# Performance work log

Measured on AMD Instinct MI355X. Metric: run time of the kernel, lower is better.

## Reference

```python
import jax, jax.numpy as jnp
import numpy as np

N_NODES = 50000
N_EDGES = 1600000
F_IN = 128
F_OUT = 64
K_ATT = 4


def setup_inputs() -> dict:
    key = jax.random.key(0)
    ks = jax.random.split(key, 12)
    s_in = 1.0 / np.sqrt(F_IN)
    s_2o = 1.0 / np.sqrt(2 * F_OUT)
    x = jax.random.normal(ks[0], (N_NODES, F_IN), dtype=jnp.float32)
    src = jax.random.randint(ks[1], (N_EDGES,), 0, N_NODES)
    dst = jax.random.randint(ks[2], (N_EDGES,), 0, N_NODES)
    Wv = jax.random.normal(ks[3], (F_IN, F_OUT), dtype=jnp.float32) * s_in
    bv = jnp.zeros((F_OUT,), dtype=jnp.float32)
    Wn = jax.random.normal(ks[4], (F_IN, F_OUT), dtype=jnp.float32) * s_in
    bn = jnp.zeros((F_OUT,), dtype=jnp.float32)
    Wt = jax.random.normal(ks[5], (K_ATT, F_IN, F_OUT), dtype=jnp.float32) * s_in
    bt = jnp.zeros((K_ATT, F_OUT), dtype=jnp.float32)
    Wa = jax.random.normal(ks[6], (K_ATT, 2 * F_OUT, F_OUT), dtype=jnp.float32) * s_2o
    ba = jnp.zeros((K_ATT, F_OUT), dtype=jnp.float32)
    return {"x": x, "src": src, "dst": dst, "Wv": Wv, "bv": bv,
            "Wn": Wn, "bn": bn, "Wt": Wt, "bt": bt, "Wa": Wa, "ba": ba}


def _forward(x, src, dst, Wv, bv, Wn, bn, Wt, bt, Wa, ba):
    N = x.shape[0]
    k = Wt.shape[0]
    out = Wv.shape[1]
    # multi-head attention logits, accumulated over heads (mean over k heads)
    att_edge = jnp.zeros((src.shape[0], out), dtype=x.dtype)
    att_self = jnp.zeros((N, out), dtype=x.dtype)
    for i in range(k):  # small fixed head count
        t = x @ Wt[i] + bt[i]                       # [N, out]
        pair_e = jnp.concatenate([t[dst], t[src]], axis=-1)  # [E, 2*out]
        att_edge = att_edge + jax.nn.relu(pair_e @ Wa[i] + ba[i])
        pair_s = jnp.concatenate([t, t], axis=-1)            # [N, 2*out]
        att_self = att_self + jax.nn.relu(pair_s @ Wa[i] + ba[i])
    att_edge = att_edge / k
    att_self = att_self / k
    e_edge = jnp.exp(att_edge)   # [E, out]
    e_self = jnp.exp(att_self)   # [N, out]
    denom = e_self + jax.ops.segment_sum(e_edge, dst, num_segments=N)
    m_self = x @ Wv + bv                  # self message  [N, out]
    m_nb = x[src] @ Wn + bn               # neighbor msgs [E, out]
    num = e_self * m_self + jax.ops.segment_sum(e_edge * m_nb, dst, num_segments=N)
    return jax.nn.relu(num / denom)


def reference(x, src, dst, Wv, bv, Wn, bn, Wt, bt, Wa, ba):
    return _forward(x, src, dst, Wv, bv, Wn, bn, Wt, bt, Wa, ba)
```

## Files before the change

### kernel.cpp

```cpp
#include <hip/hip_runtime.h>
#include <hip/hip_fp16.h>
#include <cstdint>
#include <cstddef>

#define F_IN 128
#define F_OUT 64
#define KH 4
#define CHUNK 4096
#define CAP 12800

typedef _Float16 v8h __attribute__((ext_vector_type(8)));
typedef _Float16 h2v __attribute__((ext_vector_type(2)));
typedef float v4f __attribute__((ext_vector_type(4)));
typedef float v2f __attribute__((ext_vector_type(2)));


__global__ __launch_bounds__(256) void k_part(const int* __restrict__ src,
                                              const int* __restrict__ dst,
                                              int* __restrict__ gcnt,
                                              int* __restrict__ ppack, int E){
  __shared__ int h[256];
  __shared__ int cur[256];
  const int b = blockIdx.x, t = threadIdx.x;
  h[t] = 0; __syncthreads();
  const int base = b*CHUNK;
  #pragma unroll
  for (int it = 0; it < 16; ++it){
    int i = base + it*256 + t;
    if (i < E) atomicAdd(&h[dst[i] >> 8], 1);
  }
  __syncthreads();
  if (h[t] > 0) cur[t] = t*CAP + atomicAdd(&gcnt[t], h[t]);
  __syncthreads();
  #pragma unroll
  for (int it = 0; it < 16; ++it){
    int i = base + it*256 + t;
    if (i < E){
      int d = dst[i];
      int p = atomicAdd(&cur[d >> 8], 1);
      ppack[p] = src[i] | ((d & 255) << 16);
    }
  }
}

__global__ __launch_bounds__(256) void k_fine(const int* __restrict__ ppack,
                                              const int* __restrict__ gcnt,
                                              int* __restrict__ ssrc,
                                              int* __restrict__ beg,
                                              int* __restrict__ endv, int N){
  __shared__ int s_pk[CAP];
  __shared__ int hist[256];
  __shared__ int cur[256];
  const int bkt = blockIdx.x, t = threadIdx.x;
  const int cnt = min(gcnt[bkt], CAP);
  const int b0 = bkt*CAP;
  hist[t] = 0; __syncthreads();
  for (int i = t; i < cnt; i += 256){
    int pk = ppack[b0 + i];
    atomicAdd(&hist[pk >> 16], 1);
    s_pk[i] = pk;
  }
  __syncthreads();
  int v = hist[t];
  cur[t] = v; __syncthreads();
  for (int d = 1; d < 256; d <<= 1){
    int tmp = (t >= d) ? cur[t-d] : 0;
    __syncthreads(); cur[t] += tmp; __syncthreads();
  }
  int excl = cur[t] - v;
  int node = bkt*256 + t;
  if (node < N){ beg[node] = b0 + excl; endv[node] = b0 + excl + v; }
  __syncthreads();
  cur[t] = b0 + excl;
  __syncthreads();
  for (int i = t; i < cnt; i += 256){
    int pk = s_pk[i];
    int p = atomicAdd(&cur[pk >> 16], 1);
    ssrc[p] = pk & 0xFFFF;
  }
}


__device__ __forceinline__ size_t frag_idx(int k, int col){
  int p = col >> 7, n = col & 127;
  int nt = n >> 4, nn = n & 15;
  int kc = k >> 5, q = (k >> 3) & 3, j = k & 7;
  return ((((size_t)(p*8 + nt)*4 + kc)*64) + (nn + q*16))*8 + j;
}

__global__ __launch_bounds__(256) void k_fuse(
  const float* __restrict__ Wt, const float* __restrict__ bt,
  const float* __restrict__ Wa, const float* __restrict__ ba,
  const float* __restrict__ Wv, const float* __restrict__ bv,
  const float* __restrict__ Wn, const float* __restrict__ bn,
  __half* __restrict__ Wfrag, float* __restrict__ bbig)
{
  const int b = blockIdx.x;
  const int t = threadIdx.x;

  if (b >= 8){
    int idx = (b-8)*256 + t;
    int r = idx >> 6, c = idx & 63;
    int colms = 512 + (c&7)*16 + (c>>3);
    int colh  = 512 + (c&7)*16 + 8 + (c>>3);
    Wfrag[frag_idx(r, colms)] = __float2half_rn(Wv[r*64 + c]);
    Wfrag[frag_idx(r, colh)]  = __float2half_rn(Wn[r*64 + c]);
    if (idx < 64){
      bbig[512 + (idx&7)*16 + (idx>>3)]     = bv[idx];
      bbig[512 + (idx&7)*16 + 8 + (idx>>3)] = bn[idx];
    }
    return;
  }

  __shared__ float WaH[64*65];
  const int i = b >> 1, half = b & 1;
  const int c = t & 63, w = t >> 6;

  for (int it = 0; it < 16; ++it){
    int idx = it*256 + t;
    int j = idx >> 6, cc = idx & 63;
    WaH[j*65 + cc] = Wa[i*8192 + (half*64 + j)*64 + cc];
  }
  __syncthreads();

  const int cl = c & 31;
  const int col = (c>>5)*128 + ((cl&1)*4 + i)*16 + (cl>>1) + (half ? 256 : 0);

  if (w == 0){
    const float4* bt4 = (const float4*)(bt + i*64);
    float bias = (half == 0) ? ba[i*64 + c] : 0.f;
    #pragma unroll
    for (int j4 = 0; j4 < 16; ++j4){
      float4 bv4 = bt4[j4];
      bias = fmaf(bv4.x, WaH[(j4*4+0)*65 + c], bias);
      bias = fmaf(bv4.y, WaH[(j4*4+1)*65 + c], bias);
      bias = fmaf(bv4.z, WaH[(j4*4+2)*65 + c], bias);
      bias = fmaf(bv4.w, WaH[(j4*4+3)*65 + c], bias);
    }
    bbig[col] = bias;
  }

  for (int s = 0; s < 32; ++s){
    int r = w*32 + s;
    const float4* wtr = (const float4*)(Wt + i*8192 + r*64);
    float acc = 0.f;
    #pragma unroll
    for (int j4 = 0; j4 < 16; ++j4){
      float4 w4 = wtr[j4];
      acc = fmaf(w4.x, WaH[(j4*4+0)*65 + c], acc);
      acc = fmaf(w4.y, WaH[(j4*4+1)*65 + c], acc);
      acc = fmaf(w4.z, WaH[(j4*4+2)*65 + c], acc);
      acc = fmaf(w4.w, WaH[(j4*4+3)*65 + c], acc);
    }
    Wfrag[frag_idx(r, col)] = __float2half_rn(acc);
  }
}


__global__ __launch_bounds__(256, 4) void k_gemm(
  const float* __restrict__ x, const __half* __restrict__ Wfrag,
  const float* __restrict__ bbig,
  __half* __restrict__ UMS, unsigned char* __restrict__ VH, int N)
{
  __shared__ __half Wl[16384];
  const int t = threadIdx.x;
  const int l = t & 63;
  const int w = __builtin_amdgcn_readfirstlane(t >> 6);
  const int q = l >> 4;
  const int nn = l & 15;
  const int mbase = blockIdx.x*64 + w*16;
  const int m = mbase + nn;
  const int mm = min(m, N-1);

  v8h a[4];
  const float4* xp = (const float4*)(x + (size_t)mm*128);
  #pragma unroll
  for (int kc = 0; kc < 4; ++kc){
    float4 f0 = xp[kc*8 + q*2 + 0];
    float4 f1 = xp[kc*8 + q*2 + 1];
    v8h av;
    av[0]=(_Float16)f0.x; av[1]=(_Float16)f0.y; av[2]=(_Float16)f0.z; av[3]=(_Float16)f0.w;
    av[4]=(_Float16)f1.x; av[5]=(_Float16)f1.y; av[6]=(_Float16)f1.z; av[7]=(_Float16)f1.w;
    a[kc] = av;
  }

  const v8h* Bl = (const v8h*)Wl;

  for (int p = 0; p < 5; ++p){
    __syncthreads();
    {
      const float4* sp = (const float4*)(Wfrag + (size_t)p*16384);
      float4* dp = (float4*)Wl;
      #pragma unroll
      for (int it = 0; it < 8; ++it) dp[it*256 + t] = sp[it*256 + t];
    }
    __syncthreads();

    v4f acc[8];
    #pragma unroll
    for (int nt = 0; nt < 8; ++nt){
      v4f ac = {0.f, 0.f, 0.f, 0.f};
      ac = __builtin_amdgcn_mfma_f32_16x16x32_f16(a[0], Bl[(nt*4+0)*64 + l], ac, 0,0,0);
      ac = __builtin_amdgcn_mfma_f32_16x16x32_f16(a[1], Bl[(nt*4+1)*64 + l], ac, 0,0,0);
      ac = __builtin_amdgcn_mfma_f32_16x16x32_f16(a[2], Bl[(nt*4+2)*64 + l], ac, 0,0,0);
      ac = __builtin_amdgcn_mfma_f32_16x16x32_f16(a[3], Bl[(nt*4+3)*64 + l], ac, 0,0,0);
      acc[nt] = ac;
    }

    float bbv[8];
    #pragma unroll
    for (int nt = 0; nt < 8; ++nt) bbv[nt] = bbig[p*128 + nt*16 + nn];

    #pragma unroll
    for (int r = 0; r < 4; ++r){
      int node = mbase + q*4 + r;
      if (node >= N) continue;
      float vv[8];
      #pragma unroll
      for (int nt = 0; nt < 8; ++nt) vv[nt] = acc[nt][r] + bbv[nt];

      if (p < 2){
        union { float4 f; __half h[8]; } O;
        #pragma unroll
        for (int nt = 0; nt < 8; ++nt) O.h[nt] = __float2half_rn(vv[nt]);
        __half* dstp = UMS + (size_t)node*320 + p*128 + nn*8;
        *(float4*)dstp = O.f;
      } else if (p < 4){
        int w0 = 0, w1 = 0;
        w0 = __builtin_amdgcn_cvt_pk_fp8_f32(vv[0], vv[1], w0, false);
        w0 = __builtin_amdgcn_cvt_pk_fp8_f32(vv[2], vv[3], w0, true);
        w1 = __builtin_amdgcn_cvt_pk_fp8_f32(vv[4], vv[5], w1, false);
        w1 = __builtin_amdgcn_cvt_pk_fp8_f32(vv[6], vv[7], w1, true);
        int2 pkd = make_int2(w0, w1);
        *(int2*)(VH + (size_t)node*384 + (p-2)*128 + nn*8) = pkd;
      } else {
        union { float4 f; __half h[8]; } O;
        #pragma unroll
        for (int nt = 0; nt < 8; ++nt) O.h[nt] = __float2half_rn(vv[nt]);
        if (nn < 8)
          *(float4*)(UMS + (size_t)node*320 + 256 + nn*8) = O.f;
        else
          *(float4*)(VH + (size_t)node*384 + 256 + (nn-8)*16) = O.f;
      }
    }
  }
}


__device__ __forceinline__ float elogit8(float u0,float u1,float u2,float u3, int vd){
  v2f p01 = __builtin_amdgcn_cvt_pk_f32_fp8(vd, false);
  v2f p23 = __builtin_amdgcn_cvt_pk_f32_fp8(vd, true);
  return fmaxf(u0+p01[0],0.f) + fmaxf(u1+p01[1],0.f)
       + fmaxf(u2+p23[0],0.f) + fmaxf(u3+p23[1],0.f);
}

__global__ __launch_bounds__(256) void k_edge(
  const __half* __restrict__ UMS, const unsigned char* __restrict__ VH,
  const int* __restrict__ beg, const int* __restrict__ endv,
  const int* __restrict__ ssrc,
  float* __restrict__ out, int N)
{
  int gid = blockIdx.x * 256 + threadIdx.x;
  int n = __builtin_amdgcn_readfirstlane(gid >> 6);
  int c = threadIdx.x & 63;
  if (n >= N) return;

  const float2* __restrict__ U2 = (const float2*)UMS;

  float u0, u1, u2, u3;
  {
    union { float2 f; __half2 h[2]; } U; U.f = U2[(size_t)n*80 + c];
    u0 = __low2float(U.h[0]); u1 = __high2float(U.h[0]);
    u2 = __low2float(U.h[1]); u3 = __high2float(U.h[1]);
  }
  float ms = __half2float(UMS[(size_t)n*320 + 256 + c]);

  const size_t vo = (size_t)c*4;
  const size_t ho = 256 + (size_t)c*2;

  float num, den;
  {
    int vd = *(const int*)(VH + (size_t)n*384 + vo);
    float es = __expf(0.25f * elogit8(u0,u1,u2,u3, vd));
    den = es; num = es * ms;
  }

  int j = beg[n], end = endv[n];
  for (; j + 16 <= end; j += 16){
    int vd[16]; __half hv[16];
    #pragma unroll
    for (int e = 0; e < 16; ++e){
      int s = ssrc[j+e];
      const unsigned char* r = VH + (size_t)s*384;
      vd[e] = *(const int*)(r + vo);
      hv[e] = *(const __half*)(r + ho);
    }
    float ad = 0.f, an = 0.f;
    #pragma unroll
    for (int e = 0; e < 16; ++e){
      float ee = __expf(0.25f * elogit8(u0,u1,u2,u3, vd[e]));
      ad += ee;
      an = fmaf(ee, __half2float(hv[e]), an);
    }
    den += ad; num += an;
  }
  for (; j + 4 <= end; j += 4){
    int vd[4]; __half hv[4];
    #pragma unroll
    for (int e = 0; e < 4; ++e){
      int s = ssrc[j+e];
      const unsigned char* r = VH + (size_t)s*384;
      vd[e] = *(const int*)(r + vo);
      hv[e] = *(const __half*)(r + ho);
    }
    float ad = 0.f, an = 0.f;
    #pragma unroll
    for (int e = 0; e < 4; ++e){
      float ee = __expf(0.25f * elogit8(u0,u1,u2,u3, vd[e]));
      ad += ee;
      an = fmaf(ee, __half2float(hv[e]), an);
    }
    den += ad; num += an;
  }
  for (; j < end; ++j){
    int s = ssrc[j];
    const unsigned char* r = VH + (size_t)s*384;
    int vdv = *(const int*)(r + vo);
    float hvv = __half2float(*(const __half*)(r + ho));
    float ee = __expf(0.25f * elogit8(u0,u1,u2,u3, vdv));
    den += ee;
    num = fmaf(ee, hvv, num);
  }
  out[(size_t)n*64 + c] = fmaxf(num/den, 0.f);
}


extern "C" void kernel_launch(void* const* d_in, const int* in_sizes, int n_in,
                              void* d_out, int out_size, void* d_ws, size_t ws_size,
                              hipStream_t stream)
{
  const float* x  = (const float*)d_in[0];
  const int*   src= (const int*)d_in[1];
  const int*   dst= (const int*)d_in[2];
  const float* Wv = (const float*)d_in[3];
  const float* bv = (const float*)d_in[4];
  const float* Wn = (const float*)d_in[5];
  const float* bn = (const float*)d_in[6];
  const float* Wt = (const float*)d_in[7];
  const float* bt = (const float*)d_in[8];
  const float* Wa = (const float*)d_in[9];
  const float* ba = (const float*)d_in[10];
  float* out = (float*)d_out;

  const int N = in_sizes[0] / F_IN;
  const int E = in_sizes[1];
  const int MP = ((N + 63)/64)*64;
  const int NBLK  = (E + CHUNK - 1)/CHUNK;
  const int NBUCK = (N + 255) >> 8;

  __half* Wfrag = (__half*)d_ws;
  float*  bbig  = (float*)(Wfrag + 81920);
  __half* UMS   = (__half*)(bbig + 640);
  unsigned char* VH = (unsigned char*)(UMS + (size_t)N*320);
  int*    gcnt  = (int*)(VH + (size_t)N*384);
  int*    beg   = gcnt + NBUCK;
  int*    endv  = beg + N;
  int*    ppack = endv + N;
  int*    ssrc  = ppack + (size_t)NBUCK*CAP;

  (void)hipMemsetAsync(gcnt, 0, (size_t)NBUCK*sizeof(int), stream);
  k_part<<<NBLK, 256, 0, stream>>>(src, dst, gcnt, ppack, E);
  k_fine<<<NBUCK, 256, 0, stream>>>(ppack, gcnt, ssrc, beg, endv, N);

  k_fuse<<<40, 256, 0, stream>>>(Wt, bt, Wa, ba, Wv, bv, Wn, bn, Wfrag, bbig);
  k_gemm<<<MP/64, 256, 0, stream>>>(x, Wfrag, bbig, UMS, VH, N);

  k_edge<<<(N+3)/4, 256, 0, stream>>>(UMS, VH, beg, endv, ssrc, out, N);
}
```

Baseline: 257.8 us.

## Merge CSR build kernels with weight-fuse and GEMM kernels, fold exp scale

Measured after the change: 237.3 us. -7.9%, faster.

```diff
diff --git a/kernel.cpp b/kernel.cpp
--- a/kernel.cpp
+++ b/kernel.cpp
@@ -7,78 +7,13 @@
 #define F_OUT 64
 #define KH 4
 #define CHUNK 4096
-#define CAP 12800
+#define CAP 9500
+#define NFUSE 40
+#define SCL 0.360673760222240f
 
 typedef _Float16 v8h __attribute__((ext_vector_type(8)));
-typedef _Float16 h2v __attribute__((ext_vector_type(2)));
 typedef float v4f __attribute__((ext_vector_type(4)));
 typedef float v2f __attribute__((ext_vector_type(2)));
-
-
-__global__ __launch_bounds__(256) void k_part(const int* __restrict__ src,
-                                              const int* __restrict__ dst,
-                                              int* __restrict__ gcnt,
-                                              int* __restrict__ ppack, int E){
-  __shared__ int h[256];
-  __shared__ int cur[256];
-  const int b = blockIdx.x, t = threadIdx.x;
-  h[t] = 0; __syncthreads();
-  const int base = b*CHUNK;
-  #pragma unroll
-  for (int it = 0; it < 16; ++it){
-    int i = base + it*256 + t;
-    if (i < E) atomicAdd(&h[dst[i] >> 8], 1);
-  }
-  __syncthreads();
-  if (h[t] > 0) cur[t] = t*CAP + atomicAdd(&gcnt[t], h[t]);
-  __syncthreads();
-  #pragma unroll
-  for (int it = 0; it < 16; ++it){
-    int i = base + it*256 + t;
-    if (i < E){
-      int d = dst[i];
-      int p = atomicAdd(&cur[d >> 8], 1);
-      ppack[p] = src[i] | ((d & 255) << 16);
-    }
-  }
-}
-
-__global__ __launch_bounds__(256) void k_fine(const int* __restrict__ ppack,
-                                              const int* __restrict__ gcnt,
-                                              int* __restrict__ ssrc,
-                                              int* __restrict__ beg,
-                                              int* __restrict__ endv, int N){
-  __shared__ int s_pk[CAP];
-  __shared__ int hist[256];
-  __shared__ int cur[256];
-  const int bkt = blockIdx.x, t = threadIdx.x;
-  const int cnt = min(gcnt[bkt], CAP);
-  const int b0 = bkt*CAP;
-  hist[t] = 0; __syncthreads();
-  for (int i = t; i < cnt; i += 256){
-    int pk = ppack[b0 + i];
-    atomicAdd(&hist[pk >> 16], 1);
-    s_pk[i] = pk;
-  }
-  __syncthreads();
-  int v = hist[t];
-  cur[t] = v; __syncthreads();
-  for (int d = 1; d < 256; d <<= 1){
-    int tmp = (t >= d) ? cur[t-d] : 0;
-    __syncthreads(); cur[t] += tmp; __syncthreads();
-  }
-  int excl = cur[t] - v;
-  int node = bkt*256 + t;
-  if (node < N){ beg[node] = b0 + excl; endv[node] = b0 + excl + v; }
-  __syncthreads();
-  cur[t] = b0 + excl;
-  __syncthreads();
-  for (int i = t; i < cnt; i += 256){
-    int pk = s_pk[i];
-    int p = atomicAdd(&cur[pk >> 16], 1);
-    ssrc[p] = pk & 0xFFFF;
-  }
-}
 
 
 __device__ __forceinline__ size_t frag_idx(int k, int col){
@@ -88,16 +23,54 @@
   return ((((size_t)(p*8 + nt)*4 + kc)*64) + (nn + q*16))*8 + j;
 }
 
-__global__ __launch_bounds__(256) void k_fuse(
+
+__global__ __launch_bounds__(256) void k_pre(
   const float* __restrict__ Wt, const float* __restrict__ bt,
   const float* __restrict__ Wa, const float* __restrict__ ba,
   const float* __restrict__ Wv, const float* __restrict__ bv,
   const float* __restrict__ Wn, const float* __restrict__ bn,
-  __half* __restrict__ Wfrag, float* __restrict__ bbig)
+  __half* __restrict__ Wfrag, float* __restrict__ bbig,
+  const int* __restrict__ src, const int* __restrict__ dst,
+  int* __restrict__ gcnt, int* __restrict__ ppack, int E)
 {
-  const int b = blockIdx.x;
+  __shared__ __align__(16) union {
+    float WaH[64*65];
+    struct { int h[256]; int cur[256]; } pt;
+  } sm;
+
+  const int blk = blockIdx.x;
   const int t = threadIdx.x;
 
+  if (blk >= NFUSE){
+    const int b = blk - NFUSE;
+    sm.pt.h[t] = 0; __syncthreads();
+    const int base = b*CHUNK;
+    #pragma unroll
+    for (int it = 0; it < 16; ++it){
+      int i = base + it*256 + t;
+      if (i < E) atomicAdd(&sm.pt.h[dst[i] >> 8], 1);
+    }
+    __syncthreads();
+    int hv = sm.pt.h[t];
+    if (hv > 0){
+      int bs = atomicAdd(&gcnt[t], hv);
+      if (bs + hv > CAP) bs = max(0, CAP - hv);
+      sm.pt.cur[t] = t*CAP + bs;
+    }
+    __syncthreads();
+    #pragma unroll
+    for (int it = 0; it < 16; ++it){
+      int i = base + it*256 + t;
+      if (i < E){
+        int d = dst[i];
+        int p = atomicAdd(&sm.pt.cur[d >> 8], 1);
+        ppack[p] = src[i] | ((d & 255) << 16);
+      }
+    }
+    return;
+  }
+
+  const int b = blk;
   if (b >= 8){
     int idx = (b-8)*256 + t;
     int r = idx >> 6, c = idx & 63;
@@ -112,14 +85,13 @@
     return;
   }
 
-  __shared__ float WaH[64*65];
   const int i = b >> 1, half = b & 1;
   const int c = t & 63, w = t >> 6;
 
   for (int it = 0; it < 16; ++it){
     int idx = it*256 + t;
     int j = idx >> 6, cc = idx & 63;
-    WaH[j*65 + cc] = Wa[i*8192 + (half*64 + j)*64 + cc];
+    sm.WaH[j*65 + cc] = Wa[i*8192 + (half*64 + j)*64 + cc];
   }
   __syncthreads();
 
@@ -132,12 +104,12 @@
     #pragma unroll
     for (int j4 = 0; j4 < 16; ++j4){
       float4 bv4 = bt4[j4];
-      bias = fmaf(bv4.x, WaH[(j4*4+0)*65 + c], bias);
-      bias = fmaf(bv4.y, WaH[(j4*4+1)*65 + c], bias);
-      bias = fmaf(bv4.z, WaH[(j4*4+2)*65 + c], bias);
-      bias = fmaf(bv4.w, WaH[(j4*4+3)*65 + c], bias);
-    }
-    bbig[col] = bias;
+      bias = fmaf(bv4.x, sm.WaH[(j4*4+0)*65 + c], bias);
+      bias = fmaf(bv4.y, sm.WaH[(j4*4+1)*65 + c], bias);
+      bias = fmaf(bv4.z, sm.WaH[(j4*4+2)*65 + c], bias);
+      bias = fmaf(bv4.w, sm.WaH[(j4*4+3)*65 + c], bias);
+    }
+    bbig[col] = bias * SCL;
   }
 
   for (int s = 0; s < 32; ++s){
@@ -147,28 +119,68 @@
     #pragma unroll
     for (int j4 = 0; j4 < 16; ++j4){
       float4 w4 = wtr[j4];
-      acc = fmaf(w4.x, WaH[(j4*4+0)*65 + c], acc);
-      acc = fmaf(w4.y, WaH[(j4*4+1)*65 + c], acc);
-      acc = fmaf(w4.z, WaH[(j4*4+2)*65 + c], acc);
-      acc = fmaf(w4.w, WaH[(j4*4+3)*65 + c], acc);
-    }
-    Wfrag[frag_idx(r, col)] = __float2half_rn(acc);
-  }
-}
-
-
-__global__ __launch_bounds__(256, 4) void k_gemm(
+      acc = fmaf(w4.x, sm.WaH[(j4*4+0)*65 + c], acc);
+      acc = fmaf(w4.y, sm.WaH[(j4*4+1)*65 + c], acc);
+      acc = fmaf(w4.z, sm.WaH[(j4*4+2)*65 + c], acc);
+      acc = fmaf(w4.w, sm.WaH[(j4*4+3)*65 + c], acc);
+    }
+    Wfrag[frag_idx(r, col)] = __float2half_rn(acc * SCL);
+  }
+}
+
+
+__global__ __launch_bounds__(256, 4) void k_main(
+  const int* __restrict__ ppack, const int* __restrict__ gcnt,
+  int* __restrict__ ssrc, int* __restrict__ beg, int* __restrict__ endv,
   const float* __restrict__ x, const __half* __restrict__ Wfrag,
   const float* __restrict__ bbig,
-  __half* __restrict__ UMS, unsigned char* __restrict__ VH, int N)
+  __half* __restrict__ UMS, unsigned char* __restrict__ VH,
+  int N, int NBUCK)
 {
-  __shared__ __half Wl[16384];
+  __shared__ __align__(16) union {
+    __half Wl[16384];
+    struct { int s_pk[CAP]; int hist[256]; int cur[256]; } f;
+  } sm;
+
+  const int blk = blockIdx.x;
   const int t = threadIdx.x;
+
+  if (blk < NBUCK){
+    const int bkt = blk;
+    const int cnt = min(gcnt[bkt], CAP);
+    const int b0 = bkt*CAP;
+    sm.f.hist[t] = 0; __syncthreads();
+    for (int i = t; i < cnt; i += 256){
+      int pk = ppack[b0 + i];
+      atomicAdd(&sm.f.hist[pk >> 16], 1);
+      sm.f.s_pk[i] = pk;
+    }
+    __syncthreads();
+    int v = sm.f.hist[t];
+    sm.f.cur[t] = v; __syncthreads();
+    for (int d = 1; d < 256; d <<= 1){
+      int tmp = (t >= d) ? sm.f.cur[t-d] : 0;
+      __syncthreads(); sm.f.cur[t] += tmp; __syncthreads();
+    }
+    int excl = sm.f.cur[t] - v;
+    int node = bkt*256 + t;
+    if (node < N){ beg[node] = b0 + excl; endv[node] = b0 + excl + v; }
+    __syncthreads();
+    sm.f.cur[t] = b0 + excl;
+    __syncthreads();
+    for (int i = t; i < cnt; i += 256){
+      int pk = sm.f.s_pk[i];
+      int p = atomicAdd(&sm.f.cur[pk >> 16], 1);
+      ssrc[p] = pk & 0xFFFF;
+    }
+    return;
+  }
+
   const int l = t & 63;
   const int w = __builtin_amdgcn_readfirstlane(t >> 6);
   const int q = l >> 4;
   const int nn = l & 15;
-  const int mbase = blockIdx.x*64 + w*16;
+  const int mbase = (blk - NBUCK)*64 + w*16;
   const int m = mbase + nn;
   const int mm = min(m, N-1);
 
@@ -184,13 +196,13 @@
     a[kc] = av;
   }
 
-  const v8h* Bl = (const v8h*)Wl;
+  const v8h* Bl = (const v8h*)sm.Wl;
 
   for (int p = 0; p < 5; ++p){
     __syncthreads();
     {
       const float4* sp = (const float4*)(Wfrag + (size_t)p*16384);
-      float4* dp = (float4*)Wl;
+      float4* dp = (float4*)sm.Wl;
       #pragma unroll
       for (int it = 0; it < 8; ++it) dp[it*256 + t] = sp[it*256 + t];
     }
@@ -223,8 +235,7 @@
         union { float4 f; __half h[8]; } O;
         #pragma unroll
         for (int nt = 0; nt < 8; ++nt) O.h[nt] = __float2half_rn(vv[nt]);
-        __half* dstp = UMS + (size_t)node*320 + p*128 + nn*8;
-        *(float4*)dstp = O.f;
+        *(float4*)(UMS + (size_t)node*320 + p*128 + nn*8) = O.f;
       } else if (p < 4){
         int w0 = 0, w1 = 0;
         w0 = __builtin_amdgcn_cvt_pk_fp8_f32(vv[0], vv[1], w0, false);
@@ -281,7 +292,7 @@
   float num, den;
   {
     int vd = *(const int*)(VH + (size_t)n*384 + vo);
-    float es = __expf(0.25f * elogit8(u0,u1,u2,u3, vd));
+    float es = exp2f(elogit8(u0,u1,u2,u3, vd));
     den = es; num = es * ms;
   }
 
@@ -298,7 +309,7 @@
     float ad = 0.f, an = 0.f;
     #pragma unroll
     for (int e = 0; e < 16; ++e){
-      float ee = __expf(0.25f * elogit8(u0,u1,u2,u3, vd[e]));
+      float ee = exp2f(elogit8(u0,u1,u2,u3, vd[e]));
       ad += ee;
       an = fmaf(ee, __half2float(hv[e]), an);
     }
@@ -316,7 +327,7 @@
     float ad = 0.f, an = 0.f;
     #pragma unroll
     for (int e = 0; e < 4; ++e){
-      float ee = __expf(0.25f * elogit8(u0,u1,u2,u3, vd[e]));
+      float ee = exp2f(elogit8(u0,u1,u2,u3, vd[e]));
       ad += ee;
       an = fmaf(ee, __half2float(hv[e]), an);
     }
@@ -327,7 +338,7 @@
     const unsigned char* r = VH + (size_t)s*384;
     int vdv = *(const int*)(r + vo);
     float hvv = __half2float(*(const __half*)(r + ho));
-    float ee = __expf(0.25f * elogit8(u0,u1,u2,u3, vdv));
+    float ee = exp2f(elogit8(u0,u1,u2,u3, vdv));
     den += ee;
     num = fmaf(ee, hvv, num);
   }
@@ -369,11 +380,9 @@
   int*    ssrc  = ppack + (size_t)NBUCK*CAP;
 
   (void)hipMemsetAsync(gcnt, 0, (size_t)NBUCK*sizeof(int), stream);
-  k_part<<<NBLK, 256, 0, stream>>>(src, dst, gcnt, ppack, E);
-  k_fine<<<NBUCK, 256, 0, stream>>>(ppack, gcnt, ssrc, beg, endv, N);
-
-  k_fuse<<<40, 256, 0, stream>>>(Wt, bt, Wa, ba, Wv, bv, Wn, bn, Wfrag, bbig);
-  k_gemm<<<MP/64, 256, 0, stream>>>(x, Wfrag, bbig, UMS, VH, N);
-
+  k_pre <<<NFUSE + NBLK, 256, 0, stream>>>(Wt, bt, Wa, ba, Wv, bv, Wn, bn,
+                                           Wfrag, bbig, src, dst, gcnt, ppack, E);
+  k_main<<<NBUCK + MP/64, 256, 0, stream>>>(ppack, gcnt, ssrc, beg, endv,
+                                            x, Wfrag, bbig, UMS, VH, N, NBUCK);
   k_edge<<<(N+3)/4, 256, 0, stream>>>(UMS, VH, beg, endv, ssrc, out, N);
 }
```

## Fuse pipeline stages into a cooperative persistent kernel with grid syncs

Applied to the files above, without the earlier changes.

New measurement: 276.9 us. 1.07x slower.

```diff
diff --git a/kernel.cpp b/kernel.cpp
--- a/kernel.cpp
+++ b/kernel.cpp
@@ -1,84 +1,21 @@
 #include <hip/hip_runtime.h>
 #include <hip/hip_fp16.h>
+#include <hip/hip_cooperative_groups.h>
 #include <cstdint>
 #include <cstddef>
 
+namespace cg = cooperative_groups;
+
 #define F_IN 128
-#define F_OUT 64
 #define KH 4
 #define CHUNK 4096
-#define CAP 12800
+#define CAP 9500
+#define NFUSE 40
+#define SCL 0.360673760222240f
 
 typedef _Float16 v8h __attribute__((ext_vector_type(8)));
-typedef _Float16 h2v __attribute__((ext_vector_type(2)));
 typedef float v4f __attribute__((ext_vector_type(4)));
 typedef float v2f __attribute__((ext_vector_type(2)));
-
-
-__global__ __launch_bounds__(256) void k_part(const int* __restrict__ src,
-                                              const int* __restrict__ dst,
-                                              int* __restrict__ gcnt,
-                                              int* __restrict__ ppack, int E){
-  __shared__ int h[256];
-  __shared__ int cur[256];
-  const int b = blockIdx.x, t = threadIdx.x;
-  h[t] = 0; __syncthreads();
-  const int base = b*CHUNK;
-  #pragma unroll
-  for (int it = 0; it < 16; ++it){
-    int i = base + it*256 + t;
-    if (i < E) atomicAdd(&h[dst[i] >> 8], 1);
-  }
-  __syncthreads();
-  if (h[t] > 0) cur[t] = t*CAP + atomicAdd(&gcnt[t], h[t]);
-  __syncthreads();
-  #pragma unroll
-  for (int it = 0; it < 16; ++it){
-    int i = base + it*256 + t;
-    if (i < E){
-      int d = dst[i];
-      int p = atomicAdd(&cur[d >> 8], 1);
-      ppack[p] = src[i] | ((d & 255) << 16);
-    }
-  }
-}
-
-__global__ __launch_bounds__(256) void k_fine(const int* __restrict__ ppack,
-                                              const int* __restrict__ gcnt,
-                                              int* __restrict__ ssrc,
-                                              int* __restrict__ beg,
-                                              int* __restrict__ endv, int N){
-  __shared__ int s_pk[CAP];
-  __shared__ int hist[256];
-  __shared__ int cur[256];
-  const int bkt = blockIdx.x, t = threadIdx.x;
-  const int cnt = min(gcnt[bkt], CAP);
-  const int b0 = bkt*CAP;
-  hist[t] = 0; __syncthreads();
-  for (int i = t; i < cnt; i += 256){
-    int pk = ppack[b0 + i];
-    atomicAdd(&hist[pk >> 16], 1);
-    s_pk[i] = pk;
-  }
-  __syncthreads();
-  int v = hist[t];
-  cur[t] = v; __syncthreads();
-  for (int d = 1; d < 256; d <<= 1){
-    int tmp = (t >= d) ? cur[t-d] : 0;
-    __syncthreads(); cur[t] += tmp; __syncthreads();
-  }
-  int excl = cur[t] - v;
-  int node = bkt*256 + t;
-  if (node < N){ beg[node] = b0 + excl; endv[node] = b0 + excl + v; }
-  __syncthreads();
-  cur[t] = b0 + excl;
-  __syncthreads();
-  for (int i = t; i < cnt; i += 256){
-    int pk = s_pk[i];
-    int p = atomicAdd(&cur[pk >> 16], 1);
-    ssrc[p] = pk & 0xFFFF;
-  }
-}
 
 
 __device__ __forceinline__ size_t frag_idx(int k, int col){
@@ -88,16 +25,14 @@
   return ((((size_t)(p*8 + nt)*4 + kc)*64) + (nn + q*16))*8 + j;
 }
 
-__global__ __launch_bounds__(256) void k_fuse(
+
+__device__ void do_fuse(int b, int t, float* WaH,
   const float* __restrict__ Wt, const float* __restrict__ bt,
   const float* __restrict__ Wa, const float* __restrict__ ba,
   const float* __restrict__ Wv, const float* __restrict__ bv,
   const float* __restrict__ Wn, const float* __restrict__ bn,
   __half* __restrict__ Wfrag, float* __restrict__ bbig)
 {
-  const int b = blockIdx.x;
-  const int t = threadIdx.x;
-
   if (b >= 8){
     int idx = (b-8)*256 + t;
     int r = idx >> 6, c = idx & 63;
@@ -112,7 +47,6 @@
     return;
   }
 
-  __shared__ float WaH[64*65];
   const int i = b >> 1, half = b & 1;
   const int c = t & 63, w = t >> 6;
 
@@ -137,7 +71,7 @@
       bias = fmaf(bv4.z, WaH[(j4*4+2)*65 + c], bias);
       bias = fmaf(bv4.w, WaH[(j4*4+3)*65 + c], bias);
     }
-    bbig[col] = bias;
+    bbig[col] = bias * SCL;
   }
 
   for (int s = 0; s < 32; ++s){
@@ -152,23 +86,82 @@
       acc = fmaf(w4.z, WaH[(j4*4+2)*65 + c], acc);
       acc = fmaf(w4.w, WaH[(j4*4+3)*65 + c], acc);
     }
-    Wfrag[frag_idx(r, col)] = __float2half_rn(acc);
-  }
-}
-
-
-__global__ __launch_bounds__(256, 4) void k_gemm(
+    Wfrag[frag_idx(r, col)] = __float2half_rn(acc * SCL);
+  }
+}
+
+__device__ void do_part(int b, int t, int* h, int* cur,
+  const int* __restrict__ src, const int* __restrict__ dst,
+  int* __restrict__ gcnt, int* __restrict__ ppack, int E)
+{
+  h[t] = 0; __syncthreads();
+  const int base = b*CHUNK;
+  #pragma unroll
+  for (int it = 0; it < 16; ++it){
+    int i = base + it*256 + t;
+    if (i < E) atomicAdd(&h[dst[i] >> 8], 1);
+  }
+  __syncthreads();
+  int hv = h[t];
+  if (hv > 0){
+    int bs = atomicAdd(&gcnt[t], hv);
+    if (bs + hv > CAP) bs = max(0, CAP - hv);
+    cur[t] = t*CAP + bs;
+  }
+  __syncthreads();
+  #pragma unroll
+  for (int it = 0; it < 16; ++it){
+    int i = base + it*256 + t;
+    if (i < E){
+      int d = dst[i];
+      int p = atomicAdd(&cur[d >> 8], 1);
+      ppack[p] = src[i] | ((d & 255) << 16);
+    }
+  }
+}
+
+__device__ void do_fine(int bkt, int t, int* s_pk, int* hist, int* cur,
+  const int* __restrict__ ppack, const int* __restrict__ gcnt,
+  int* __restrict__ ssrc, int* __restrict__ beg, int* __restrict__ endv, int N)
+{
+  const int cnt = min(gcnt[bkt], CAP);
+  const int b0 = bkt*CAP;
+  hist[t] = 0; __syncthreads();
+  for (int i = t; i < cnt; i += 256){
+    int pk = ppack[b0 + i];
+    atomicAdd(&hist[pk >> 16], 1);
+    s_pk[i] = pk;
+  }
+  __syncthreads();
+  int v = hist[t];
+  cur[t] = v; __syncthreads();
+  for (int d = 1; d < 256; d <<= 1){
+    int tmp = (t >= d) ? cur[t-d] : 0;
+    __syncthreads(); cur[t] += tmp; __syncthreads();
+  }
+  int excl = cur[t] - v;
+  int node = bkt*256 + t;
+  if (node < N){ beg[node] = b0 + excl; endv[node] = b0 + excl + v; }
+  __syncthreads();
+  cur[t] = b0 + excl;
+  __syncthreads();
+  for (int i = t; i < cnt; i += 256){
+    int pk = s_pk[i];
+    int p = atomicAdd(&cur[pk >> 16], 1);
+    ssrc[p] = pk & 0xFFFF;
+  }
+}
+
+__device__ void do_gemm(int gb, int t, __half* Wl,
   const float* __restrict__ x, const __half* __restrict__ Wfrag,
   const float* __restrict__ bbig,
   __half* __restrict__ UMS, unsigned char* __restrict__ VH, int N)
 {
-  __shared__ __half Wl[16384];
-  const int t = threadIdx.x;
   const int l = t & 63;
   const int w = __builtin_amdgcn_readfirstlane(t >> 6);
   const int q = l >> 4;
   const int nn = l & 15;
-  const int mbase = blockIdx.x*64 + w*16;
+  const int mbase = gb*64 + w*16;
   const int m = mbase + nn;
   const int mm = min(m, N-1);
 
@@ -223,8 +216,7 @@
         union { float4 f; __half h[8]; } O;
         #pragma unroll
         for (int nt = 0; nt < 8; ++nt) O.h[nt] = __float2half_rn(vv[nt]);
-        __half* dstp = UMS + (size_t)node*320 + p*128 + nn*8;
-        *(float4*)dstp = O.f;
+        *(float4*)(UMS + (size_t)node*320 + p*128 + nn*8) = O.f;
       } else if (p < 4){
         int w0 = 0, w1 = 0;
         w0 = __builtin_amdgcn_cvt_pk_fp8_f32(vv[0], vv[1], w0, false);
@@ -246,7 +238,6 @@
   }
 }
 
-
 __device__ __forceinline__ float elogit8(float u0,float u1,float u2,float u3, int vd){
   v2f p01 = __builtin_amdgcn_cvt_pk_f32_fp8(vd, false);
   v2f p23 = __builtin_amdgcn_cvt_pk_f32_fp8(vd, true);
@@ -254,15 +245,13 @@
        + fmaxf(u2+p23[0],0.f) + fmaxf(u3+p23[1],0.f);
 }
 
-__global__ __launch_bounds__(256) void k_edge(
+__device__ void do_edge(int g, int t,
   const __half* __restrict__ UMS, const unsigned char* __restrict__ VH,
   const int* __restrict__ beg, const int* __restrict__ endv,
-  const int* __restrict__ ssrc,
-  float* __restrict__ out, int N)
-{
-  int gid = blockIdx.x * 256 + threadIdx.x;
-  int n = __builtin_amdgcn_readfirstlane(gid >> 6);
-  int c = threadIdx.x & 63;
+  const int* __restrict__ ssrc, float* __restrict__ out, int N)
+{
+  int n = __builtin_amdgcn_readfirstlane(g*4 + (t >> 6));
+  int c = t & 63;
   if (n >= N) return;
 
   const float2* __restrict__ U2 = (const float2*)UMS;
@@ -281,7 +270,7 @@
   float num, den;
   {
     int vd = *(const int*)(VH + (size_t)n*384 + vo);
-    float es = __expf(0.25f * elogit8(u0,u1,u2,u3, vd));
+    float es = exp2f(elogit8(u0,u1,u2,u3, vd));
     den = es; num = es * ms;
   }
 
@@ -298,7 +287,7 @@
     float ad = 0.f, an = 0.f;
     #pragma unroll
     for (int e = 0; e < 16; ++e){
-      float ee = __expf(0.25f * elogit8(u0,u1,u2,u3, vd[e]));
+      float ee = exp2f(elogit8(u0,u1,u2,u3, vd[e]));
       ad += ee;
       an = fmaf(ee, __half2float(hv[e]), an);
     }
@@ -316,7 +305,7 @@
     float ad = 0.f, an = 0.f;
     #pragma unroll
     for (int e = 0; e < 4; ++e){
-      float ee = __expf(0.25f * elogit8(u0,u1,u2,u3, vd[e]));
+      float ee = exp2f(elogit8(u0,u1,u2,u3, vd[e]));
       ad += ee;
       an = fmaf(ee, __half2float(hv[e]), an);
     }
@@ -327,11 +316,75 @@
     const unsigned char* r = VH + (size_t)s*384;
     int vdv = *(const int*)(r + vo);
     float hvv = __half2float(*(const __half*)(r + ho));
-    float ee = __expf(0.25f * elogit8(u0,u1,u2,u3, vdv));
+    float ee = exp2f(elogit8(u0,u1,u2,u3, vdv));
     den += ee;
     num = fmaf(ee, hvv, num);
   }
   out[(size_t)n*64 + c] = fmaxf(num/den, 0.f);
+}
+
+
+struct MegaArgs {
+  const float* x; const int* src; const int* dst;
+  const float *Wt,*bt,*Wa,*ba,*Wv,*bv,*Wn,*bn;
+  __half* Wfrag; float* bbig; __half* UMS; unsigned char* VH;
+  int* gcnt; int* beg; int* endv; int* ppack; int* ssrc;
+  float* out; int N; int E; int NBLK; int NBUCK; int NGEMM; int NEDGE;
+};
+
+union SMU {
+  float WaH[64*65];
+  struct { int h[256]; int cur[256]; } pt;
+  struct { int s_pk[CAP]; int hist[256]; int cur[256]; } f;
+  __half Wl[16384];
+};
+
+__global__ __launch_bounds__(256, 4) void k_mega(MegaArgs A)
+{
+  __shared__ __align__(16) SMU sm;
+  const int t = threadIdx.x;
+  cg::grid_group grid = cg::this_grid();
+
+  for (int u = blockIdx.x; u < NFUSE + A.NBLK; u += gridDim.x){
+    if (u < NFUSE) do_fuse(u, t, sm.WaH, A.Wt,A.bt,A.Wa,A.ba,A.Wv,A.bv,A.Wn,A.bn,
+                           A.Wfrag, A.bbig);
+    else           do_part(u - NFUSE, t, sm.pt.h, sm.pt.cur, A.src, A.dst,
+                           A.gcnt, A.ppack, A.E);
+    __syncthreads();
+  }
+  grid.sync();
+
+  for (int u = blockIdx.x; u < A.NBUCK + A.NGEMM; u += gridDim.x){
+    if (u < A.NBUCK) do_fine(u, t, sm.f.s_pk, sm.f.hist, sm.f.cur, A.ppack, A.gcnt,
+                             A.ssrc, A.beg, A.endv, A.N);
+    else             do_gemm(u - A.NBUCK, t, sm.Wl, A.x, A.Wfrag, A.bbig,
+                             A.UMS, A.VH, A.N);
+    __syncthreads();
+  }
+  grid.sync();
+
+  for (int g = blockIdx.x; g < A.NEDGE; g += gridDim.x)
+    do_edge(g, t, A.UMS, A.VH, A.beg, A.endv, A.ssrc, A.out, A.N);
+}
+
+
+__global__ __launch_bounds__(256) void k_pre(MegaArgs A){
+  __shared__ __align__(16) union { float WaH[64*65]; struct { int h[256]; int cur[256]; } pt; } sm;
+  const int blk = blockIdx.x, t = threadIdx.x;
+  if (blk < NFUSE) do_fuse(blk, t, sm.WaH, A.Wt,A.bt,A.Wa,A.ba,A.Wv,A.bv,A.Wn,A.bn, A.Wfrag, A.bbig);
+  else             do_part(blk - NFUSE, t, sm.pt.h, sm.pt.cur, A.src, A.dst, A.gcnt, A.ppack, A.E);
+}
+
+__global__ __launch_bounds__(256, 4) void k_main(MegaArgs A){
+  __shared__ __align__(16) SMU sm;
+  const int blk = blockIdx.x, t = threadIdx.x;
+  if (blk < A.NBUCK) do_fine(blk, t, sm.f.s_pk, sm.f.hist, sm.f.cur, A.ppack, A.gcnt,
+                             A.ssrc, A.beg, A.endv, A.N);
+  else               do_gemm(blk - A.NBUCK, t, sm.Wl, A.x, A.Wfrag, A.bbig, A.UMS, A.VH, A.N);
+}
+
+__global__ __launch_bounds__(256) void k_edge(MegaArgs A){
+  do_edge(blockIdx.x, threadIdx.x, A.UMS, A.VH, A.beg, A.endv, A.ssrc, A.out, A.N);
 }
 
 
@@ -342,15 +395,6 @@
   const float* x  = (const float*)d_in[0];
   const int*   src= (const int*)d_in[1];
   const int*   dst= (const int*)d_in[2];
-  const float* Wv = (const float*)d_in[3];
-  const float* bv = (const float*)d_in[4];
-  const float* Wn = (const float*)d_in[5];
-  const float* bn = (const float*)d_in[6];
-  const float* Wt = (const float*)d_in[7];
-  const float* bt = (const float*)d_in[8];
-  const float* Wa = (const float*)d_in[9];
-  const float* ba = (const float*)d_in[10];
-  float* out = (float*)d_out;
 
   const int N = in_sizes[0] / F_IN;
   const int E = in_sizes[1];
@@ -368,12 +412,34 @@
   int*    ppack = endv + N;
   int*    ssrc  = ppack + (size_t)NBUCK*CAP;
 
+  MegaArgs ha;
+  ha.x = x; ha.src = src; ha.dst = dst;
+  ha.Wt = (const float*)d_in[7];  ha.bt = (const float*)d_in[8];
+  ha.Wa = (const float*)d_in[9];  ha.ba = (const float*)d_in[10];
+  ha.Wv = (const float*)d_in[3];  ha.bv = (const float*)d_in[4];
+  ha.Wn = (const float*)d_in[5];  ha.bn = (const float*)d_in[6];
+  ha.Wfrag = Wfrag; ha.bbig = bbig; ha.UMS = UMS; ha.VH = VH;
+  ha.gcnt = gcnt; ha.beg = beg; ha.endv = endv; ha.ppack = ppack; ha.ssrc = ssrc;
+  ha.out = (float*)d_out;
+  ha.N = N; ha.E = E; ha.NBLK = NBLK; ha.NBUCK = NBUCK;
+  ha.NGEMM = MP/64; ha.NEDGE = (N + 3)/4;
+
   (void)hipMemsetAsync(gcnt, 0, (size_t)NBUCK*sizeof(int), stream);
-  k_part<<<NBLK, 256, 0, stream>>>(src, dst, gcnt, ppack, E);
-  k_fine<<<NBUCK, 256, 0, stream>>>(ppack, gcnt, ssrc, beg, endv, N);
-
-  k_fuse<<<40, 256, 0, stream>>>(Wt, bt, Wa, ba, Wv, bv, Wn, bn, Wfrag, bbig);
-  k_gemm<<<MP/64, 256, 0, stream>>>(x, Wfrag, bbig, UMS, VH, N);
-
-  k_edge<<<(N+3)/4, 256, 0, stream>>>(UMS, VH, beg, endv, ssrc, out, N);
-}
+
+  int maxb = 0;
+  hipError_t oe = hipOccupancyMaxActiveBlocksPerMultiprocessor(&maxb, k_mega, 256, 0);
+  bool coop_ok = false;
+  if (oe == hipSuccess && maxb > 0){
+    int grid = maxb * 256;
+    if (grid > 1024) grid = 1024;
+    void* params[] = { (void*)&ha };
+    hipError_t le = hipLaunchCooperativeKernel((const void*)k_mega, dim3(grid),
+                                               dim3(256), params, 0u, stream);
+    coop_ok = (le == hipSuccess);
+  }
+  if (!coop_ok){
+    k_pre <<<NFUSE + NBLK, 256, 0, stream>>>(ha);
+    k_main<<<NBUCK + MP/64, 256, 0, stream>>>(ha);
+    k_edge<<<(N+3)/4, 256, 0, stream>>>(ha);
+  }
+}
```
